# Performance work log

Hardware: AMD Instinct MI355X
Metric: run time of the kernel (lower is better)

The kernel has to match this reference:

```python
import jax, jax.numpy as jnp
import numpy as np

N_NODES = 100000
N_EDGES = 1600000


def _degree_norms(src, dst, n):
    ones = jnp.ones(src.shape[0], dtype=jnp.float32)
    deg_out = jax.ops.segment_sum(ones, src, num_segments=n)
    deg_in = jax.ops.segment_sum(ones, dst, num_segments=n)
    src_norm = jax.lax.rsqrt(jnp.maximum(deg_out, 1.0))
    dst_norm = jax.lax.rsqrt(jnp.maximum(deg_in, 1.0))
    return src_norm, dst_norm


def _graph_conv(x, W, b, src, dst, src_norm, dst_norm, n):
    # DGL GraphConv, norm='both': D_dst^{-1/2} A D_src^{-1/2} X W + b
    # Apply W first (same math, smaller messages).
    h = x @ W                                  # [N, out]
    m = (h * src_norm[:, None])[src]           # [E, out] gather
    agg = jax.ops.segment_sum(m, dst, num_segments=n)  # [N, out] scatter-add
    return agg * dst_norm[:, None] + b


def setup_inputs() -> dict:
    key = jax.random.key(0)
    ks = jax.random.split(key, 10)
    inp = {
        "x": jax.random.normal(ks[0], (N_NODES, 128), dtype=jnp.float32),
        "src": jax.random.randint(ks[1], (N_EDGES,), 0, N_NODES, dtype=jnp.int32),
        "dst": jax.random.randint(ks[2], (N_EDGES,), 0, N_NODES, dtype=jnp.int32),
        "W1": jax.random.normal(ks[3], (128, 64), dtype=jnp.float32) * 0.08,
        "b1": jnp.zeros((64,), dtype=jnp.float32),
        "W2": jax.random.normal(ks[4], (64, 64), dtype=jnp.float32) * 0.12,
        "b2": jnp.zeros((64,), dtype=jnp.float32),
        "W3": jax.random.normal(ks[5], (64, 64), dtype=jnp.float32) * 0.12,
        "b3": jnp.zeros((64,), dtype=jnp.float32),
        "W4": jax.random.normal(ks[6], (64, 64), dtype=jnp.float32) * 0.12,
        "b4": jnp.zeros((64,), dtype=jnp.float32),
        "Wres": jax.random.normal(ks[7], (128, 64), dtype=jnp.float32) * 0.08,
        "bres": jnp.zeros((64,), dtype=jnp.float32),
        "Wop": jax.random.normal(ks[8], (64, 16), dtype=jnp.float32) * 0.12,
        "bop": jnp.zeros((16,), dtype=jnp.float32),
    }
    return inp


def reference(x, src, dst, W1, b1, W2, b2, W3, b3, W4, b4, Wres, bres, Wop, bop):
    n = x.shape[0]
    src_norm, dst_norm = _degree_norms(src, dst, n)
    res = x @ Wres + bres
    out = jax.nn.relu(_graph_conv(x, W1, b1, src, dst, src_norm, dst_norm, n))
    out = jax.nn.relu(_graph_conv(out, W2, b2, src, dst, src_norm, dst_norm, n))
    out = jax.nn.relu(_graph_conv(out, W3, b3, src, dst, src_norm, dst_norm, n))
    out = _graph_conv(out, W4, b4, src, dst, src_norm, dst_norm, n)
    out = jax.nn.relu(out + res)
    return out @ Wop + bop
```

## Files before the change

### kernel.cpp

```cpp
#include <hip/hip_runtime.h>
#include <cstdint>
#include <cstddef>


#define SLOTS 64
#define BCAP 5120
#define ACHUNK 4096

__device__ __forceinline__ unsigned short f2bf(float f) {
  union { float f; unsigned u; } v; v.f = f;
  unsigned r = (v.u + 0x7fffu + ((v.u >> 16) & 1u)) >> 16;
  return (unsigned short)r;
}
__device__ __forceinline__ float bf2f(unsigned short h) {
  union { unsigned u; float f; } v; v.u = ((unsigned)h) << 16;
  return v.f;
}
__device__ __forceinline__ void bf2x2(unsigned u, float* lo, float* hi) {
  union { unsigned x; float f; } a, b;
  a.x = u << 16; b.x = u & 0xFFFF0000u;
  *lo = a.f; *hi = b.f;
}

__global__ __launch_bounds__(256) void bucket_kernel(
    const int* __restrict__ src, const int* __restrict__ dst,
    int* __restrict__ gcur_d, int* __restrict__ gcur_s,
    unsigned* __restrict__ dbuck, unsigned char* __restrict__ sbuck,
    int E, int nbuck) {
  __shared__ int s_src[ACHUNK];
  __shared__ int s_dst[ACHUNK];
  __shared__ int run_d[512];
  __shared__ int run_s[512];
  const int t = threadIdx.x;
  const int base = blockIdx.x * ACHUNK;
  int cnt = E - base;
  if (cnt > ACHUNK) cnt = ACHUNK;

  for (int i = t; i < cnt; i += 256) {
    s_src[i] = src[base + i];
    s_dst[i] = dst[base + i];
  }
  for (int i = t; i < nbuck; i += 256) { run_d[i] = 0; run_s[i] = 0; }
  __syncthreads();
  for (int i = t; i < cnt; i += 256) {
    atomicAdd(&run_d[s_dst[i] >> 8], 1);
    atomicAdd(&run_s[s_src[i] >> 8], 1);
  }
  __syncthreads();
  {
    const int iters = (nbuck + 255) >> 8;
    for (int it = 0; it < iters; ++it) {
      int i = it * 256 + t;
      int hd = 0, hs = 0;
      if (i < nbuck) { hd = run_d[i]; hs = run_s[i]; }
      __syncthreads();
      if (i < nbuck) {
        run_d[i] = hd ? atomicAdd(&gcur_d[i], hd) : 0;
        run_s[i] = hs ? atomicAdd(&gcur_s[i], hs) : 0;
      }
      __syncthreads();
    }
  }
  for (int i = t; i < cnt; i += 256) {
    int d = s_dst[i], s = s_src[i];
    int bd = d >> 8;
    int pd = atomicAdd(&run_d[bd], 1);
    if (pd < BCAP) dbuck[(size_t)bd * BCAP + pd] = ((unsigned)(d & 255) << 24) | (unsigned)s;
    int bs = s >> 8;
    int ps = atomicAdd(&run_s[bs], 1);
    if (ps < BCAP) sbuck[(size_t)bs * BCAP + ps] = (unsigned char)(s & 255);
  }
}

__global__ __launch_bounds__(256) void csr_kernel(
    const unsigned* __restrict__ dbuck, const int* __restrict__ gcur_d,
    int* __restrict__ col, int* __restrict__ cnt_arr,
    float* __restrict__ dnorm, int N) {
  __shared__ int cur[256];
  const int b = blockIdx.x;
  const int t = threadIdx.x;
  const int node0 = b << 8;
  cur[t] = 0;
  __syncthreads();
  int cnt = gcur_d[b];
  if (cnt > BCAP) cnt = BCAP;
  const unsigned* p = dbuck + (size_t)b * BCAP;
  for (int i = t; i < cnt; i += 256) {
    unsigned e = p[i];
    int nl = e >> 24;
    int s = (int)(e & 0x00FFFFFFu);
    int pos = atomicAdd(&cur[nl], 1);
    if (pos < SLOTS) col[(size_t)(node0 + nl) * SLOTS + pos] = s;
  }
  __syncthreads();
  int node = node0 + t;
  if (node < N) {
    int c = cur[t];
    cnt_arr[node] = c;
    float d = (float)(c < 1 ? 1 : c);
    dnorm[node] = rsqrtf(d);
  }
}

__global__ __launch_bounds__(256) void degout_kernel(
    const unsigned char* __restrict__ sbuck, const int* __restrict__ gcur_s,
    float* __restrict__ snorm, int N) {
  __shared__ int cur[256];
  const int b = blockIdx.x;
  const int t = threadIdx.x;
  cur[t] = 0;
  __syncthreads();
  int cnt = gcur_s[b];
  if (cnt > BCAP) cnt = BCAP;
  const unsigned char* p = sbuck + (size_t)b * BCAP;
  for (int i = t; i < cnt; i += 256) atomicAdd(&cur[p[i]], 1);
  __syncthreads();
  int node = (b << 8) + t;
  if (node < N) {
    int c = cur[t];
    snorm[node] = rsqrtf((float)(c < 1 ? 1 : c));
  }
}

#define GEMM_STEP(r, aval, wv)                   \
  acc[r][0] = fmaf((aval), (wv).x, acc[r][0]);   \
  acc[r][1] = fmaf((aval), (wv).y, acc[r][1]);   \
  acc[r][2] = fmaf((aval), (wv).z, acc[r][2]);   \
  acc[r][3] = fmaf((aval), (wv).w, acc[r][3]);

#define GEMM_INNER_LOOP                                        \
  for (int kc = 0; kc < 64; kc += 4) {                         \
    float4 a0 = *(const float4*)&in_lds[ty4 + 0][kc];          \
    float4 a1 = *(const float4*)&in_lds[ty4 + 1][kc];          \
    float4 a2 = *(const float4*)&in_lds[ty4 + 2][kc];          \
    float4 a3 = *(const float4*)&in_lds[ty4 + 3][kc];          \
    float4 w0 = *(const float4*)&w_lds[kc + 0][tx4];           \
    float4 w1 = *(const float4*)&w_lds[kc + 1][tx4];           \
    float4 w2 = *(const float4*)&w_lds[kc + 2][tx4];           \
    float4 w3 = *(const float4*)&w_lds[kc + 3][tx4];           \
    GEMM_STEP(0, a0.x, w0) GEMM_STEP(0, a0.y, w1) GEMM_STEP(0, a0.z, w2) GEMM_STEP(0, a0.w, w3) \
    GEMM_STEP(1, a1.x, w0) GEMM_STEP(1, a1.y, w1) GEMM_STEP(1, a1.z, w2) GEMM_STEP(1, a1.w, w3) \
    GEMM_STEP(2, a2.x, w0) GEMM_STEP(2, a2.y, w1) GEMM_STEP(2, a2.z, w2) GEMM_STEP(2, a2.w, w3) \
    GEMM_STEP(3, a3.x, w0) GEMM_STEP(3, a3.y, w1) GEMM_STEP(3, a3.z, w2) GEMM_STEP(3, a3.w, w3) \
  }

template <int K>
__global__ __launch_bounds__(256) void gemm_f32_kernel(
    const float* __restrict__ X, const float* __restrict__ W,
    const float* __restrict__ norm, unsigned short* __restrict__ out, int n) {
  __shared__ float in_lds[64][68];
  __shared__ float w_lds[64][64];
  const int t = threadIdx.x;
  const int tx4 = (t & 15) * 4;
  const int ty4 = (t >> 4) * 4;
  const int node0 = blockIdx.x * 64;
  const int srow = t >> 2;
  const int scol = (t & 3) * 16;

  float acc[4][4];
#pragma unroll
  for (int r = 0; r < 4; r++)
#pragma unroll
    for (int j = 0; j < 4; j++) acc[r][j] = 0.f;

  for (int kb = 0; kb < K; kb += 64) {
    {
      int gi = node0 + srow;
      float4 v0, v1, v2, v3;
      if (gi < n) {
        const float* s = X + (size_t)gi * K + kb + scol;
        v0 = *(const float4*)(s + 0);
        v1 = *(const float4*)(s + 4);
        v2 = *(const float4*)(s + 8);
        v3 = *(const float4*)(s + 12);
      } else {
        v0 = v1 = v2 = v3 = make_float4(0.f, 0.f, 0.f, 0.f);
      }
      *(float4*)&in_lds[srow][scol + 0]  = v0;
      *(float4*)&in_lds[srow][scol + 4]  = v1;
      *(float4*)&in_lds[srow][scol + 8]  = v2;
      *(float4*)&in_lds[srow][scol + 12] = v3;
    }
    {
      const float* s = W + (size_t)(kb + srow) * 64 + scol;
      float4 w0 = *(const float4*)(s + 0);
      float4 w1 = *(const float4*)(s + 4);
      float4 w2 = *(const float4*)(s + 8);
      float4 w3 = *(const float4*)(s + 12);
      *(float4*)&w_lds[srow][scol + 0]  = w0;
      *(float4*)&w_lds[srow][scol + 4]  = w1;
      *(float4*)&w_lds[srow][scol + 8]  = w2;
      *(float4*)&w_lds[srow][scol + 12] = w3;
    }
    __syncthreads();
    GEMM_INNER_LOOP
    __syncthreads();
  }

#pragma unroll
  for (int r = 0; r < 4; r++) {
    int gi = node0 + ty4 + r;
    if (gi >= n) continue;
    float s = norm[gi];
    ushort4 o;
    o.x = f2bf(acc[r][0] * s);
    o.y = f2bf(acc[r][1] * s);
    o.z = f2bf(acc[r][2] * s);
    o.w = f2bf(acc[r][3] * s);
    *(ushort4*)&out[(size_t)gi * 64 + tx4] = o;
  }
}

__global__ __launch_bounds__(256) void gemm_bf16_kernel(
    const unsigned short* __restrict__ X, const float* __restrict__ W,
    const float* __restrict__ norm, unsigned short* __restrict__ out, int n) {
  __shared__ float in_lds[64][68];
  __shared__ float w_lds[64][64];
  const int t = threadIdx.x;
  const int tx4 = (t & 15) * 4;
  const int ty4 = (t >> 4) * 4;
  const int node0 = blockIdx.x * 64;
  const int srow = t >> 2;
  const int scol = (t & 3) * 16;

  float acc[4][4];
#pragma unroll
  for (int r = 0; r < 4; r++)
#pragma unroll
    for (int j = 0; j < 4; j++) acc[r][j] = 0.f;

  {
    int gi = node0 + srow;
    float f[16];
    if (gi < n) {
      const unsigned short* s = X + (size_t)gi * 64 + scol;
      uint4 u0 = *(const uint4*)(s + 0);
      uint4 u1 = *(const uint4*)(s + 8);
      bf2x2(u0.x, &f[0], &f[1]);   bf2x2(u0.y, &f[2], &f[3]);
      bf2x2(u0.z, &f[4], &f[5]);   bf2x2(u0.w, &f[6], &f[7]);
      bf2x2(u1.x, &f[8], &f[9]);   bf2x2(u1.y, &f[10], &f[11]);
      bf2x2(u1.z, &f[12], &f[13]); bf2x2(u1.w, &f[14], &f[15]);
    } else {
#pragma unroll
      for (int j = 0; j < 16; j++) f[j] = 0.f;
    }
#pragma unroll
    for (int j = 0; j < 16; j += 4)
      *(float4*)&in_lds[srow][scol + j] = make_float4(f[j], f[j+1], f[j+2], f[j+3]);
  }
  {
    const float* s = W + (size_t)srow * 64 + scol;
    float4 w0 = *(const float4*)(s + 0);
    float4 w1 = *(const float4*)(s + 4);
    float4 w2 = *(const float4*)(s + 8);
    float4 w3 = *(const float4*)(s + 12);
    *(float4*)&w_lds[srow][scol + 0]  = w0;
    *(float4*)&w_lds[srow][scol + 4]  = w1;
    *(float4*)&w_lds[srow][scol + 8]  = w2;
    *(float4*)&w_lds[srow][scol + 12] = w3;
  }
  __syncthreads();
  GEMM_INNER_LOOP

#pragma unroll
  for (int r = 0; r < 4; r++) {
    int gi = node0 + ty4 + r;
    if (gi >= n) continue;
    float s = norm[gi];
    ushort4 o;
    o.x = f2bf(acc[r][0] * s);
    o.y = f2bf(acc[r][1] * s);
    o.z = f2bf(acc[r][2] * s);
    o.w = f2bf(acc[r][3] * s);
    *(ushort4*)&out[(size_t)gi * 64 + tx4] = o;
  }
}

#define UNPACK_ADD(u, A)                         \
  { float f0, f1, f2, f3;                        \
    bf2x2((u).x, &f0, &f1);                      \
    bf2x2((u).y, &f2, &f3);                      \
    A[0] += f0; A[1] += f1; A[2] += f2; A[3] += f3; }

template <int RELU>
__global__ __launch_bounds__(256) void agg_kernel(
    const unsigned short* __restrict__ H, const int* __restrict__ cnt_arr,
    const int* __restrict__ col, const float* __restrict__ dnorm,
    const float* __restrict__ bias, unsigned short* __restrict__ O,
    int n) {
  const int lane = threadIdx.x & 63;
  const int sub = lane >> 4;
  const int fl  = lane & 15;
  const int wave = (blockIdx.x * blockDim.x + threadIdx.x) >> 6;
  const int nwaves = (gridDim.x * blockDim.x) >> 6;
  const uint2* __restrict__ H2 = (const uint2*)H;
  const float4 bb = ((const float4*)bias)[fl];

  for (int v = wave; v < n; v += nwaves) {
    int cnt = cnt_arr[v];
    if (cnt > SLOTS) cnt = SLOTS;
    const size_t base = (size_t)v * SLOTS;
    int cv = (lane < cnt) ? col[base + lane] : 0;
    float accA[4] = {0.f, 0.f, 0.f, 0.f};
    float accB[4] = {0.f, 0.f, 0.f, 0.f};
    int j = 0;
    for (; j + 8 <= cnt; j += 8) {
      int c0 = __shfl(cv, j + sub);
      int c1 = __shfl(cv, j + 4 + sub);
      uint2 u0 = H2[(size_t)c0 * 16 + fl];
      uint2 u1 = H2[(size_t)c1 * 16 + fl];
      UNPACK_ADD(u0, accA)
      UNPACK_ADD(u1, accB)
    }
    for (; j < cnt; j += 4) {
      int e = j + sub;
      int c = __shfl(cv, e);
      if (e < cnt) {
        uint2 u = H2[(size_t)c * 16 + fl];
        UNPACK_ADD(u, accA)
      }
    }
#pragma unroll
    for (int i = 0; i < 4; i++) {
      float a = accA[i] + accB[i];
      a += __shfl_xor(a, 16);
      a += __shfl_xor(a, 32);
      accA[i] = a;
    }
    if (sub == 0) {
      float d = dnorm[v];
      float v0 = accA[0] * d + bb.x;
      float v1 = accA[1] * d + bb.y;
      float v2 = accA[2] * d + bb.z;
      float v3 = accA[3] * d + bb.w;
      if (RELU) {
        v0 = fmaxf(v0, 0.f); v1 = fmaxf(v1, 0.f);
        v2 = fmaxf(v2, 0.f); v3 = fmaxf(v3, 0.f);
      }
      ushort4 o;
      o.x = f2bf(v0); o.y = f2bf(v1); o.z = f2bf(v2); o.w = f2bf(v3);
      *(ushort4*)&O[base + 4 * fl] = o;
    }
  }
}

__global__ __launch_bounds__(256) void final_kernel(
    const float* __restrict__ X, const float* __restrict__ Wres,
    const float* __restrict__ bres, const unsigned short* __restrict__ O4,
    const float* __restrict__ Wop, const float* __restrict__ bop,
    float* __restrict__ out, int n) {
  __shared__ float in_lds[64][68];
  __shared__ float w_lds[64][64];
  __shared__ float wop_lds[64][16];
  const int t = threadIdx.x;
  const int tx4 = (t & 15) * 4;
  const int ty4 = (t >> 4) * 4;
  const int node0 = blockIdx.x * 64;
  const int srow = t >> 2;
  const int scol = (t & 3) * 16;

  ((float4*)&wop_lds[0][0])[t] = ((const float4*)Wop)[t];

  float acc[4][4];
#pragma unroll
  for (int r = 0; r < 4; r++)
#pragma unroll
    for (int j = 0; j < 4; j++) acc[r][j] = 0.f;

  for (int kb = 0; kb < 128; kb += 64) {
    {
      int gi = node0 + srow;
      float4 v0, v1, v2, v3;
      if (gi < n) {
        const float* s = X + (size_t)gi * 128 + kb + scol;
        v0 = *(const float4*)(s + 0);
        v1 = *(const float4*)(s + 4);
        v2 = *(const float4*)(s + 8);
        v3 = *(const float4*)(s + 12);
      } else {
        v0 = v1 = v2 = v3 = make_float4(0.f, 0.f, 0.f, 0.f);
      }
      *(float4*)&in_lds[srow][scol + 0]  = v0;
      *(float4*)&in_lds[srow][scol + 4]  = v1;
      *(float4*)&in_lds[srow][scol + 8]  = v2;
      *(float4*)&in_lds[srow][scol + 12] = v3;
    }
    {
      const float* s = Wres + (size_t)(kb + srow) * 64 + scol;
      float4 w0 = *(const float4*)(s + 0);
      float4 w1 = *(const float4*)(s + 4);
      float4 w2 = *(const float4*)(s + 8);
      float4 w3 = *(const float4*)(s + 12);
      *(float4*)&w_lds[srow][scol + 0]  = w0;
      *(float4*)&w_lds[srow][scol + 4]  = w1;
      *(float4*)&w_lds[srow][scol + 8]  = w2;
      *(float4*)&w_lds[srow][scol + 12] = w3;
    }
    __syncthreads();
    GEMM_INNER_LOOP
    __syncthreads();
  }

#pragma unroll
  for (int r = 0; r < 4; r++) {
    int gi = node0 + ty4 + r;
    float4 o = make_float4(0.f, 0.f, 0.f, 0.f);
    if (gi < n) {
      ushort4 v = *(const ushort4*)&O4[(size_t)gi * 64 + tx4];
      o.x = fmaxf(acc[r][0] + bres[tx4 + 0] + bf2f(v.x), 0.f);
      o.y = fmaxf(acc[r][1] + bres[tx4 + 1] + bf2f(v.y), 0.f);
      o.z = fmaxf(acc[r][2] + bres[tx4 + 2] + bf2f(v.z), 0.f);
      o.w = fmaxf(acc[r][3] + bres[tx4 + 3] + bf2f(v.w), 0.f);
    }
    *(float4*)&in_lds[ty4 + r][tx4] = o;
  }
  __syncthreads();

  {
    int nn = t >> 2;
    int fg = t & 3;
    float4 a = ((const float4*)bop)[fg];
#pragma unroll 16
    for (int k = 0; k < 64; k++) {
      float tv = in_lds[nn][k];
      float4 w = *(const float4*)&wop_lds[k][fg * 4];
      a.x = fmaf(tv, w.x, a.x);
      a.y = fmaf(tv, w.y, a.y);
      a.z = fmaf(tv, w.z, a.z);
      a.w = fmaf(tv, w.w, a.w);
    }
    int node = node0 + nn;
    if (node < n) *(float4*)&out[(size_t)node * 16 + fg * 4] = a;
  }
}

extern "C" void kernel_launch(void* const* d_in, const int* in_sizes, int n_in,
                              void* d_out, int out_size, void* d_ws, size_t ws_size,
                              hipStream_t stream) {
  const float* x    = (const float*)d_in[0];
  const int*   src  = (const int*)d_in[1];
  const int*   dst  = (const int*)d_in[2];
  const float* W1   = (const float*)d_in[3];
  const float* b1   = (const float*)d_in[4];
  const float* W2   = (const float*)d_in[5];
  const float* b2   = (const float*)d_in[6];
  const float* W3   = (const float*)d_in[7];
  const float* b3   = (const float*)d_in[8];
  const float* W4   = (const float*)d_in[9];
  const float* b4   = (const float*)d_in[10];
  const float* Wres = (const float*)d_in[11];
  const float* bres = (const float*)d_in[12];
  const float* Wop  = (const float*)d_in[13];
  const float* bop  = (const float*)d_in[14];
  float* out = (float*)d_out;

  const int N = in_sizes[0] / 128;
  const int E = in_sizes[1];
  const int nbuck = (N + 255) >> 8;

  char* p = (char*)d_ws;
  auto alloc = [&](size_t b) {
    char* r = p;
    p += (b + 255) & ~(size_t)255;
    return r;
  };
  int*            gcur_d  = (int*)alloc((size_t)nbuck * 4);
  int*            gcur_s  = (int*)alloc((size_t)nbuck * 4);
  unsigned*       dbuck   = (unsigned*)alloc((size_t)nbuck * BCAP * 4);
  unsigned char*  sbuck   = (unsigned char*)alloc((size_t)nbuck * BCAP);
  int*            col     = (int*)alloc((size_t)N * SLOTS * 4);
  int*            cnt_arr = (int*)alloc((size_t)N * 4);
  float*          snorm   = (float*)alloc((size_t)N * 4);
  float*          dnorm   = (float*)alloc((size_t)N * 4);
  unsigned short* Hbuf    = (unsigned short*)alloc((size_t)N * 64 * 2);
  unsigned short* Obuf    = (unsigned short*)alloc((size_t)N * 64 * 2);

  hipMemsetAsync(gcur_d, 0, (size_t)nbuck * 4, stream);
  hipMemsetAsync(gcur_s, 0, (size_t)nbuck * 4, stream);

  int ga = (E + ACHUNK - 1) / ACHUNK;
  bucket_kernel<<<ga, 256, 0, stream>>>(src, dst, gcur_d, gcur_s, dbuck, sbuck, E, nbuck);
  csr_kernel<<<nbuck, 256, 0, stream>>>(dbuck, gcur_d, col, cnt_arr, dnorm, N);
  degout_kernel<<<nbuck, 256, 0, stream>>>(sbuck, gcur_s, snorm, N);

  int gb = (N + 63) / 64;
  gemm_f32_kernel<128><<<gb, 256, 0, stream>>>(x, W1, snorm, Hbuf, N);
  agg_kernel<1><<<2048, 256, 0, stream>>>(Hbuf, cnt_arr, col, dnorm, b1, Obuf, N);
  gemm_bf16_kernel<<<gb, 256, 0, stream>>>(Obuf, W2, snorm, Hbuf, N);
  agg_kernel<1><<<2048, 256, 0, stream>>>(Hbuf, cnt_arr, col, dnorm, b2, Obuf, N);
  gemm_bf16_kernel<<<gb, 256, 0, stream>>>(Obuf, W3, snorm, Hbuf, N);
  agg_kernel<1><<<2048, 256, 0, stream>>>(Hbuf, cnt_arr, col, dnorm, b3, Obuf, N);
  gemm_bf16_kernel<<<gb, 256, 0, stream>>>(Obuf, W4, snorm, Hbuf, N);
  agg_kernel<0><<<2048, 256, 0, stream>>>(Hbuf, cnt_arr, col, dnorm, b4, Obuf, N);
  final_kernel<<<gb, 256, 0, stream>>>(x, Wres, bres, Obuf, Wop, bop, out, N);
}
```

Measured before the change: 325.7 us.

## Fuse residual GEMM into first GEMM and process two nodes per wave in aggregation

The residual projection x@Wres now happens in the first-layer GEMM kernel, which shares the x tile load with W1 and writes a bf16 residual buffer, so the final kernel no longer rereads x in fp32. The aggregation kernel now handles two destination nodes per wave and interleaves their gathers to raise memory-level parallelism. The two memsets become a single init kernel. In exchange the first GEMM uses more LDS and registers, the residual is rounded to bf16, and the aggregation loop runs to the larger of the two degrees with predicated loads.

Result: no change. 326.5 us (+0.3%).

```diff
diff --git a/kernel.cpp b/kernel.cpp
--- a/kernel.cpp
+++ b/kernel.cpp
@@ -20,6 +20,11 @@
   union { unsigned x; float f; } a, b;
   a.x = u << 16; b.x = u & 0xFFFF0000u;
   *lo = a.f; *hi = b.f;
+}
+
+__global__ void init_kernel(int* __restrict__ gcur_d, int* __restrict__ gcur_s, int nbuck) {
+  int i = blockIdx.x * blockDim.x + threadIdx.x;
+  if (i < nbuck) { gcur_d[i] = 0; gcur_s[i] = 0; }
 }
 
 __global__ __launch_bounds__(256) void bucket_kernel(
@@ -122,34 +127,41 @@
   }
 }
 
-#define GEMM_STEP(r, aval, wv)                   \
-  acc[r][0] = fmaf((aval), (wv).x, acc[r][0]);   \
-  acc[r][1] = fmaf((aval), (wv).y, acc[r][1]);   \
-  acc[r][2] = fmaf((aval), (wv).z, acc[r][2]);   \
-  acc[r][3] = fmaf((aval), (wv).w, acc[r][3]);
-
-#define GEMM_INNER_LOOP                                        \
-  for (int kc = 0; kc < 64; kc += 4) {                         \
-    float4 a0 = *(const float4*)&in_lds[ty4 + 0][kc];          \
-    float4 a1 = *(const float4*)&in_lds[ty4 + 1][kc];          \
-    float4 a2 = *(const float4*)&in_lds[ty4 + 2][kc];          \
-    float4 a3 = *(const float4*)&in_lds[ty4 + 3][kc];          \
-    float4 w0 = *(const float4*)&w_lds[kc + 0][tx4];           \
-    float4 w1 = *(const float4*)&w_lds[kc + 1][tx4];           \
-    float4 w2 = *(const float4*)&w_lds[kc + 2][tx4];           \
-    float4 w3 = *(const float4*)&w_lds[kc + 3][tx4];           \
-    GEMM_STEP(0, a0.x, w0) GEMM_STEP(0, a0.y, w1) GEMM_STEP(0, a0.z, w2) GEMM_STEP(0, a0.w, w3) \
-    GEMM_STEP(1, a1.x, w0) GEMM_STEP(1, a1.y, w1) GEMM_STEP(1, a1.z, w2) GEMM_STEP(1, a1.w, w3) \
-    GEMM_STEP(2, a2.x, w0) GEMM_STEP(2, a2.y, w1) GEMM_STEP(2, a2.z, w2) GEMM_STEP(2, a2.w, w3) \
-    GEMM_STEP(3, a3.x, w0) GEMM_STEP(3, a3.y, w1) GEMM_STEP(3, a3.z, w2) GEMM_STEP(3, a3.w, w3) \
-  }
-
-template <int K>
-__global__ __launch_bounds__(256) void gemm_f32_kernel(
-    const float* __restrict__ X, const float* __restrict__ W,
-    const float* __restrict__ norm, unsigned short* __restrict__ out, int n) {
+#define GEMM_STEP(ACC, r, aval, wv)                 \
+  ACC[r][0] = fmaf((aval), (wv).x, ACC[r][0]);      \
+  ACC[r][1] = fmaf((aval), (wv).y, ACC[r][1]);      \
+  ACC[r][2] = fmaf((aval), (wv).z, ACC[r][2]);      \
+  ACC[r][3] = fmaf((aval), (wv).w, ACC[r][3]);
+
+#define GEMM_ROW(ACC, W_LDS, kc)                                         \
+  { float4 w0 = *(const float4*)&W_LDS[kc + 0][tx4];                     \
+    float4 w1 = *(const float4*)&W_LDS[kc + 1][tx4];                     \
+    float4 w2 = *(const float4*)&W_LDS[kc + 2][tx4];                     \
+    float4 w3 = *(const float4*)&W_LDS[kc + 3][tx4];                     \
+    GEMM_STEP(ACC, 0, a0.x, w0) GEMM_STEP(ACC, 0, a0.y, w1) GEMM_STEP(ACC, 0, a0.z, w2) GEMM_STEP(ACC, 0, a0.w, w3) \
+    GEMM_STEP(ACC, 1, a1.x, w0) GEMM_STEP(ACC, 1, a1.y, w1) GEMM_STEP(ACC, 1, a1.z, w2) GEMM_STEP(ACC, 1, a1.w, w3) \
+    GEMM_STEP(ACC, 2, a2.x, w0) GEMM_STEP(ACC, 2, a2.y, w1) GEMM_STEP(ACC, 2, a2.z, w2) GEMM_STEP(ACC, 2, a2.w, w3) \
+    GEMM_STEP(ACC, 3, a3.x, w0) GEMM_STEP(ACC, 3, a3.y, w1) GEMM_STEP(ACC, 3, a3.z, w2) GEMM_STEP(ACC, 3, a3.w, w3) }
+
+#define STAGE_W_TILE(W_PTR, W_LDS)                                \
+  { const float* s_ = (W_PTR) + (size_t)srow * 64 + scol;         \
+    float4 q0 = *(const float4*)(s_ + 0);                         \
+    float4 q1 = *(const float4*)(s_ + 4);                         \
+    float4 q2 = *(const float4*)(s_ + 8);                         \
+    float4 q3 = *(const float4*)(s_ + 12);                        \
+    *(float4*)&W_LDS[srow][scol + 0]  = q0;                       \
+    *(float4*)&W_LDS[srow][scol + 4]  = q1;                       \
+    *(float4*)&W_LDS[srow][scol + 8]  = q2;                       \
+    *(float4*)&W_LDS[srow][scol + 12] = q3; }
+
+__global__ __launch_bounds__(256) void gemm1_kernel(
+    const float* __restrict__ X, const float* __restrict__ W1,
+    const float* __restrict__ Wres, const float* __restrict__ bres,
+    const float* __restrict__ norm,
+    unsigned short* __restrict__ Hout, unsigned short* __restrict__ Rout, int n) {
   __shared__ float in_lds[64][68];
   __shared__ float w_lds[64][64];
+  __shared__ float wr_lds[64][64];
   const int t = threadIdx.x;
   const int tx4 = (t & 15) * 4;
   const int ty4 = (t >> 4) * 4;
@@ -157,215 +169,11 @@
   const int srow = t >> 2;
   const int scol = (t & 3) * 16;
 
-  float acc[4][4];
+  float acc[4][4], acc2[4][4];
 #pragma unroll
   for (int r = 0; r < 4; r++)
 #pragma unroll
-    for (int j = 0; j < 4; j++) acc[r][j] = 0.f;
-
-  for (int kb = 0; kb < K; kb += 64) {
-    {
-      int gi = node0 + srow;
-      float4 v0, v1, v2, v3;
-      if (gi < n) {
-        const float* s = X + (size_t)gi * K + kb + scol;
-        v0 = *(const float4*)(s + 0);
-        v1 = *(const float4*)(s + 4);
-        v2 = *(const float4*)(s + 8);
-        v3 = *(const float4*)(s + 12);
-      } else {
-        v0 = v1 = v2 = v3 = make_float4(0.f, 0.f, 0.f, 0.f);
-      }
-      *(float4*)&in_lds[srow][scol + 0]  = v0;
-      *(float4*)&in_lds[srow][scol + 4]  = v1;
-      *(float4*)&in_lds[srow][scol + 8]  = v2;
-      *(float4*)&in_lds[srow][scol + 12] = v3;
-    }
-    {
-      const float* s = W + (size_t)(kb + srow) * 64 + scol;
-      float4 w0 = *(const float4*)(s + 0);
-      float4 w1 = *(const float4*)(s + 4);
-      float4 w2 = *(const float4*)(s + 8);
-      float4 w3 = *(const float4*)(s + 12);
-      *(float4*)&w_lds[srow][scol + 0]  = w0;
-      *(float4*)&w_lds[srow][scol + 4]  = w1;
-      *(float4*)&w_lds[srow][scol + 8]  = w2;
-      *(float4*)&w_lds[srow][scol + 12] = w3;
-    }
-    __syncthreads();
-    GEMM_INNER_LOOP
-    __syncthreads();
-  }
-
-#pragma unroll
-  for (int r = 0; r < 4; r++) {
-    int gi = node0 + ty4 + r;
-    if (gi >= n) continue;
-    float s = norm[gi];
-    ushort4 o;
-    o.x = f2bf(acc[r][0] * s);
-    o.y = f2bf(acc[r][1] * s);
-    o.z = f2bf(acc[r][2] * s);
-    o.w = f2bf(acc[r][3] * s);
-    *(ushort4*)&out[(size_t)gi * 64 + tx4] = o;
-  }
-}
-
-__global__ __launch_bounds__(256) void gemm_bf16_kernel(
-    const unsigned short* __restrict__ X, const float* __restrict__ W,
-    const float* __restrict__ norm, unsigned short* __restrict__ out, int n) {
-  __shared__ float in_lds[64][68];
-  __shared__ float w_lds[64][64];
-  const int t = threadIdx.x;
-  const int tx4 = (t & 15) * 4;
-  const int ty4 = (t >> 4) * 4;
-  const int node0 = blockIdx.x * 64;
-  const int srow = t >> 2;
-  const int scol = (t & 3) * 16;
-
-  float acc[4][4];
-#pragma unroll
-  for (int r = 0; r < 4; r++)
-#pragma unroll
-    for (int j = 0; j < 4; j++) acc[r][j] = 0.f;
-
-  {
-    int gi = node0 + srow;
-    float f[16];
-    if (gi < n) {
-      const unsigned short* s = X + (size_t)gi * 64 + scol;
-      uint4 u0 = *(const uint4*)(s + 0);
-      uint4 u1 = *(const uint4*)(s + 8);
-      bf2x2(u0.x, &f[0], &f[1]);   bf2x2(u0.y, &f[2], &f[3]);
-      bf2x2(u0.z, &f[4], &f[5]);   bf2x2(u0.w, &f[6], &f[7]);
-      bf2x2(u1.x, &f[8], &f[9]);   bf2x2(u1.y, &f[10], &f[11]);
-      bf2x2(u1.z, &f[12], &f[13]); bf2x2(u1.w, &f[14], &f[15]);
-    } else {
-#pragma unroll
-      for (int j = 0; j < 16; j++) f[j] = 0.f;
-    }
-#pragma unroll
-    for (int j = 0; j < 16; j += 4)
-      *(float4*)&in_lds[srow][scol + j] = make_float4(f[j], f[j+1], f[j+2], f[j+3]);
-  }
-  {
-    const float* s = W + (size_t)srow * 64 + scol;
-    float4 w0 = *(const float4*)(s + 0);
-    float4 w1 = *(const float4*)(s + 4);
-    float4 w2 = *(const float4*)(s + 8);
-    float4 w3 = *(const float4*)(s + 12);
-    *(float4*)&w_lds[srow][scol + 0]  = w0;
-    *(float4*)&w_lds[srow][scol + 4]  = w1;
-    *(float4*)&w_lds[srow][scol + 8]  = w2;
-    *(float4*)&w_lds[srow][scol + 12] = w3;
-  }
-  __syncthreads();
-  GEMM_INNER_LOOP
-
-#pragma unroll
-  for (int r = 0; r < 4; r++) {
-    int gi = node0 + ty4 + r;
-    if (gi >= n) continue;
-    float s = norm[gi];
-    ushort4 o;
-    o.x = f2bf(acc[r][0] * s);
-    o.y = f2bf(acc[r][1] * s);
-    o.z = f2bf(acc[r][2] * s);
-    o.w = f2bf(acc[r][3] * s);
-    *(ushort4*)&out[(size_t)gi * 64 + tx4] = o;
-  }
-}
-
-#define UNPACK_ADD(u, A)                         \
-  { float f0, f1, f2, f3;                        \
-    bf2x2((u).x, &f0, &f1);                      \
-    bf2x2((u).y, &f2, &f3);                      \
-    A[0] += f0; A[1] += f1; A[2] += f2; A[3] += f3; }
-
-template <int RELU>
-__global__ __launch_bounds__(256) void agg_kernel(
-    const unsigned short* __restrict__ H, const int* __restrict__ cnt_arr,
-    const int* __restrict__ col, const float* __restrict__ dnorm,
-    const float* __restrict__ bias, unsigned short* __restrict__ O,
-    int n) {
-  const int lane = threadIdx.x & 63;
-  const int sub = lane >> 4;
-  const int fl  = lane & 15;
-  const int wave = (blockIdx.x * blockDim.x + threadIdx.x) >> 6;
-  const int nwaves = (gridDim.x * blockDim.x) >> 6;
-  const uint2* __restrict__ H2 = (const uint2*)H;
-  const float4 bb = ((const float4*)bias)[fl];
-
-  for (int v = wave; v < n; v += nwaves) {
-    int cnt = cnt_arr[v];
-    if (cnt > SLOTS) cnt = SLOTS;
-    const size_t base = (size_t)v * SLOTS;
-    int cv = (lane < cnt) ? col[base + lane] : 0;
-    float accA[4] = {0.f, 0.f, 0.f, 0.f};
-    float accB[4] = {0.f, 0.f, 0.f, 0.f};
-    int j = 0;
-    for (; j + 8 <= cnt; j += 8) {
-      int c0 = __shfl(cv, j + sub);
-      int c1 = __shfl(cv, j + 4 + sub);
-      uint2 u0 = H2[(size_t)c0 * 16 + fl];
-      uint2 u1 = H2[(size_t)c1 * 16 + fl];
-      UNPACK_ADD(u0, accA)
-      UNPACK_ADD(u1, accB)
-    }
-    for (; j < cnt; j += 4) {
-      int e = j + sub;
-      int c = __shfl(cv, e);
-      if (e < cnt) {
-        uint2 u = H2[(size_t)c * 16 + fl];
-        UNPACK_ADD(u, accA)
-      }
-    }
-#pragma unroll
-    for (int i = 0; i < 4; i++) {
-      float a = accA[i] + accB[i];
-      a += __shfl_xor(a, 16);
-      a += __shfl_xor(a, 32);
-      accA[i] = a;
-    }
-    if (sub == 0) {
-      float d = dnorm[v];
-      float v0 = accA[0] * d + bb.x;
-      float v1 = accA[1] * d + bb.y;
-      float v2 = accA[2] * d + bb.z;
-      float v3 = accA[3] * d + bb.w;
-      if (RELU) {
-        v0 = fmaxf(v0, 0.f); v1 = fmaxf(v1, 0.f);
-        v2 = fmaxf(v2, 0.f); v3 = fmaxf(v3, 0.f);
-      }
-      ushort4 o;
-      o.x = f2bf(v0); o.y = f2bf(v1); o.z = f2bf(v2); o.w = f2bf(v3);
-      *(ushort4*)&O[base + 4 * fl] = o;
-    }
-  }
-}
-
-__global__ __launch_bounds__(256) void final_kernel(
-    const float* __restrict__ X, const float* __restrict__ Wres,
-    const float* __restrict__ bres, const unsigned short* __restrict__ O4,
-    const float* __restrict__ Wop, const float* __restrict__ bop,
-    float* __restrict__ out, int n) {
-  __shared__ float in_lds[64][68];
-  __shared__ float w_lds[64][64];
-  __shared__ float wop_lds[64][16];
-  const int t = threadIdx.x;
-  const int tx4 = (t & 15) * 4;
-  const int ty4 = (t >> 4) * 4;
-  const int node0 = blockIdx.x * 64;
-  const int srow = t >> 2;
-  const int scol = (t & 3) * 16;
-
-  ((float4*)&wop_lds[0][0])[t] = ((const float4*)Wop)[t];
-
-  float acc[4][4];
-#pragma unroll
-  for (int r = 0; r < 4; r++)
-#pragma unroll
-    for (int j = 0; j < 4; j++) acc[r][j] = 0.f;
+    for (int j = 0; j < 4; j++) { acc[r][j] = 0.f; acc2[r][j] = 0.f; }
 
   for (int kb = 0; kb < 128; kb += 64) {
     {
@@ -385,34 +193,232 @@
       *(float4*)&in_lds[srow][scol + 8]  = v2;
       *(float4*)&in_lds[srow][scol + 12] = v3;
     }
-    {
-      const float* s = Wres + (size_t)(kb + srow) * 64 + scol;
-      float4 w0 = *(const float4*)(s + 0);
-      float4 w1 = *(const float4*)(s + 4);
-      float4 w2 = *(const float4*)(s + 8);
-      float4 w3 = *(const float4*)(s + 12);
-      *(float4*)&w_lds[srow][scol + 0]  = w0;
-      *(float4*)&w_lds[srow][scol + 4]  = w1;
-      *(float4*)&w_lds[srow][scol + 8]  = w2;
-      *(float4*)&w_lds[srow][scol + 12] = w3;
-    }
+    STAGE_W_TILE(W1 + (size_t)kb * 64, w_lds)
+    STAGE_W_TILE(Wres + (size_t)kb * 64, wr_lds)
     __syncthreads();
-    GEMM_INNER_LOOP
+
+    for (int kc = 0; kc < 64; kc += 4) {
+      float4 a0 = *(const float4*)&in_lds[ty4 + 0][kc];
+      float4 a1 = *(const float4*)&in_lds[ty4 + 1][kc];
+      float4 a2 = *(const float4*)&in_lds[ty4 + 2][kc];
+      float4 a3 = *(const float4*)&in_lds[ty4 + 3][kc];
+      GEMM_ROW(acc, w_lds, kc)
+      GEMM_ROW(acc2, wr_lds, kc)
+    }
     __syncthreads();
   }
 
 #pragma unroll
   for (int r = 0; r < 4; r++) {
     int gi = node0 + ty4 + r;
-    float4 o = make_float4(0.f, 0.f, 0.f, 0.f);
+    if (gi >= n) continue;
+    float s = norm[gi];
+    ushort4 h;
+    h.x = f2bf(acc[r][0] * s);
+    h.y = f2bf(acc[r][1] * s);
+    h.z = f2bf(acc[r][2] * s);
+    h.w = f2bf(acc[r][3] * s);
+    *(ushort4*)&Hout[(size_t)gi * 64 + tx4] = h;
+    ushort4 rr;
+    rr.x = f2bf(acc2[r][0] + bres[tx4 + 0]);
+    rr.y = f2bf(acc2[r][1] + bres[tx4 + 1]);
+    rr.z = f2bf(acc2[r][2] + bres[tx4 + 2]);
+    rr.w = f2bf(acc2[r][3] + bres[tx4 + 3]);
+    *(ushort4*)&Rout[(size_t)gi * 64 + tx4] = rr;
+  }
+}
+
+__global__ __launch_bounds__(256) void gemm_bf16_kernel(
+    const unsigned short* __restrict__ X, const float* __restrict__ W,
+    const float* __restrict__ norm, unsigned short* __restrict__ out, int n) {
+  __shared__ float in_lds[64][68];
+  __shared__ float w_lds[64][64];
+  const int t = threadIdx.x;
+  const int tx4 = (t & 15) * 4;
+  const int ty4 = (t >> 4) * 4;
+  const int node0 = blockIdx.x * 64;
+  const int srow = t >> 2;
+  const int scol = (t & 3) * 16;
+
+  float acc[4][4];
+#pragma unroll
+  for (int r = 0; r < 4; r++)
+#pragma unroll
+    for (int j = 0; j < 4; j++) acc[r][j] = 0.f;
+
+  {
+    int gi = node0 + srow;
+    float f[16];
     if (gi < n) {
-      ushort4 v = *(const ushort4*)&O4[(size_t)gi * 64 + tx4];
-      o.x = fmaxf(acc[r][0] + bres[tx4 + 0] + bf2f(v.x), 0.f);
-      o.y = fmaxf(acc[r][1] + bres[tx4 + 1] + bf2f(v.y), 0.f);
-      o.z = fmaxf(acc[r][2] + bres[tx4 + 2] + bf2f(v.z), 0.f);
-      o.w = fmaxf(acc[r][3] + bres[tx4 + 3] + bf2f(v.w), 0.f);
-    }
-    *(float4*)&in_lds[ty4 + r][tx4] = o;
+      const unsigned short* s = X + (size_t)gi * 64 + scol;
+      uint4 u0 = *(const uint4*)(s + 0);
+      uint4 u1 = *(const uint4*)(s + 8);
+      bf2x2(u0.x, &f[0], &f[1]);   bf2x2(u0.y, &f[2], &f[3]);
+      bf2x2(u0.z, &f[4], &f[5]);   bf2x2(u0.w, &f[6], &f[7]);
+      bf2x2(u1.x, &f[8], &f[9]);   bf2x2(u1.y, &f[10], &f[11]);
+      bf2x2(u1.z, &f[12], &f[13]); bf2x2(u1.w, &f[14], &f[15]);
+    } else {
+#pragma unroll
+      for (int j = 0; j < 16; j++) f[j] = 0.f;
+    }
+#pragma unroll
+    for (int j = 0; j < 16; j += 4)
+      *(float4*)&in_lds[srow][scol + j] = make_float4(f[j], f[j+1], f[j+2], f[j+3]);
+  }
+  STAGE_W_TILE(W, w_lds)
+  __syncthreads();
+
+  for (int kc = 0; kc < 64; kc += 4) {
+    float4 a0 = *(const float4*)&in_lds[ty4 + 0][kc];
+    float4 a1 = *(const float4*)&in_lds[ty4 + 1][kc];
+    float4 a2 = *(const float4*)&in_lds[ty4 + 2][kc];
+    float4 a3 = *(const float4*)&in_lds[ty4 + 3][kc];
+    GEMM_ROW(acc, w_lds, kc)
+  }
+
+#pragma unroll
+  for (int r = 0; r < 4; r++) {
+    int gi = node0 + ty4 + r;
+    if (gi >= n) continue;
+    float s = norm[gi];
+    ushort4 o;
+    o.x = f2bf(acc[r][0] * s);
+    o.y = f2bf(acc[r][1] * s);
+    o.z = f2bf(acc[r][2] * s);
+    o.w = f2bf(acc[r][3] * s);
+    *(ushort4*)&out[(size_t)gi * 64 + tx4] = o;
+  }
+}
+
+#define UNPACK_ADD(u, A)                         \
+  { float f0, f1, f2, f3;                        \
+    bf2x2((u).x, &f0, &f1);                      \
+    bf2x2((u).y, &f2, &f3);                      \
+    A[0] += f0; A[1] += f1; A[2] += f2; A[3] += f3; }
+
+template <int RELU>
+__global__ __launch_bounds__(256) void agg_kernel(
+    const unsigned short* __restrict__ H, const int* __restrict__ cnt_arr,
+    const int* __restrict__ col, const float* __restrict__ dnorm,
+    const float* __restrict__ bias, unsigned short* __restrict__ O,
+    int n) {
+  const int lane = threadIdx.x & 63;
+  const int sub = lane >> 4;
+  const int fl  = lane & 15;
+  const int wave = (blockIdx.x * blockDim.x + threadIdx.x) >> 6;
+  const int nwaves = (gridDim.x * blockDim.x) >> 6;
+  const uint2* __restrict__ H2 = (const uint2*)H;
+  const float4 bb = ((const float4*)bias)[fl];
+
+  for (int v0 = wave * 2; v0 < n; v0 += nwaves * 2) {
+    const int v1 = v0 + 1;
+    int cnt0 = cnt_arr[v0];
+    int cnt1 = (v1 < n) ? cnt_arr[v1] : 0;
+    if (cnt0 > SLOTS) cnt0 = SLOTS;
+    if (cnt1 > SLOTS) cnt1 = SLOTS;
+    const size_t base0 = (size_t)v0 * SLOTS;
+    const size_t base1 = (size_t)v1 * SLOTS;
+    int cv0 = (lane < cnt0) ? col[base0 + lane] : 0;
+    int cv1 = (lane < cnt1) ? col[base1 + lane] : 0;
+    float a0[4] = {0.f, 0.f, 0.f, 0.f};
+    float b0[4] = {0.f, 0.f, 0.f, 0.f};
+    float a1[4] = {0.f, 0.f, 0.f, 0.f};
+    float b1[4] = {0.f, 0.f, 0.f, 0.f};
+    const int cmax = cnt0 > cnt1 ? cnt0 : cnt1;
+    for (int j = 0; j < cmax; j += 8) {
+      const int e0 = j + sub;
+      const int e1 = j + 4 + sub;
+      int c00 = __shfl(cv0, e0);
+      int c01 = __shfl(cv0, e1);
+      int c10 = __shfl(cv1, e0);
+      int c11 = __shfl(cv1, e1);
+      if (e0 < cnt0) { uint2 u = H2[(size_t)c00 * 16 + fl]; UNPACK_ADD(u, a0) }
+      if (e0 < cnt1) { uint2 u = H2[(size_t)c10 * 16 + fl]; UNPACK_ADD(u, a1) }
+      if (e1 < cnt0) { uint2 u = H2[(size_t)c01 * 16 + fl]; UNPACK_ADD(u, b0) }
+      if (e1 < cnt1) { uint2 u = H2[(size_t)c11 * 16 + fl]; UNPACK_ADD(u, b1) }
+    }
+    float r0[4], r1[4];
+#pragma unroll
+    for (int i = 0; i < 4; i++) {
+      float s0 = a0[i] + b0[i];
+      s0 += __shfl_xor(s0, 16);
+      s0 += __shfl_xor(s0, 32);
+      r0[i] = s0;
+      float s1 = a1[i] + b1[i];
+      s1 += __shfl_xor(s1, 16);
+      s1 += __shfl_xor(s1, 32);
+      r1[i] = s1;
+    }
+    if (sub == 0) {
+      float d = dnorm[v0];
+      float q0 = r0[0] * d + bb.x;
+      float q1 = r0[1] * d + bb.y;
+      float q2 = r0[2] * d + bb.z;
+      float q3 = r0[3] * d + bb.w;
+      if (RELU) {
+        q0 = fmaxf(q0, 0.f); q1 = fmaxf(q1, 0.f);
+        q2 = fmaxf(q2, 0.f); q3 = fmaxf(q3, 0.f);
+      }
+      ushort4 o;
+      o.x = f2bf(q0); o.y = f2bf(q1); o.z = f2bf(q2); o.w = f2bf(q3);
+      *(ushort4*)&O[base0 + 4 * fl] = o;
+    } else if (sub == 1 && v1 < n) {
+      float d = dnorm[v1];
+      float q0 = r1[0] * d + bb.x;
+      float q1 = r1[1] * d + bb.y;
+      float q2 = r1[2] * d + bb.z;
+      float q3 = r1[3] * d + bb.w;
+      if (RELU) {
+        q0 = fmaxf(q0, 0.f); q1 = fmaxf(q1, 0.f);
+        q2 = fmaxf(q2, 0.f); q3 = fmaxf(q3, 0.f);
+      }
+      ushort4 o;
+      o.x = f2bf(q0); o.y = f2bf(q1); o.z = f2bf(q2); o.w = f2bf(q3);
+      *(ushort4*)&O[base1 + 4 * fl] = o;
+    }
+  }
+}
+
+__global__ __launch_bounds__(256) void final_kernel(
+    const unsigned short* __restrict__ O4, const unsigned short* __restrict__ R,
+    const float* __restrict__ Wop, const float* __restrict__ bop,
+    float* __restrict__ out, int n) {
+  __shared__ float t_lds[64][68];
+  __shared__ float wop_lds[64][16];
+  const int t = threadIdx.x;
+  const int node0 = blockIdx.x * 64;
+  const int srow = t >> 2;
+  const int scol = (t & 3) * 16;
+
+  ((float4*)&wop_lds[0][0])[t] = ((const float4*)Wop)[t];
+
+  {
+    int gi = node0 + srow;
+    float f[16];
+    if (gi < n) {
+      const unsigned short* po = O4 + (size_t)gi * 64 + scol;
+      const unsigned short* pr = R + (size_t)gi * 64 + scol;
+      uint4 uo0 = *(const uint4*)(po + 0);
+      uint4 uo1 = *(const uint4*)(po + 8);
+      uint4 ur0 = *(const uint4*)(pr + 0);
+      uint4 ur1 = *(const uint4*)(pr + 8);
+      float o0, o1, rr0, rr1;
+#define ADDRELU2(UO, UR, idx)                         \
+      bf2x2(UO, &o0, &o1); bf2x2(UR, &rr0, &rr1);     \
+      f[idx] = fmaxf(o0 + rr0, 0.f);                  \
+      f[idx + 1] = fmaxf(o1 + rr1, 0.f);
+      ADDRELU2(uo0.x, ur0.x, 0)  ADDRELU2(uo0.y, ur0.y, 2)
+      ADDRELU2(uo0.z, ur0.z, 4)  ADDRELU2(uo0.w, ur0.w, 6)
+      ADDRELU2(uo1.x, ur1.x, 8)  ADDRELU2(uo1.y, ur1.y, 10)
+      ADDRELU2(uo1.z, ur1.z, 12) ADDRELU2(uo1.w, ur1.w, 14)
+#undef ADDRELU2
+    } else {
+#pragma unroll
+      for (int j = 0; j < 16; j++) f[j] = 0.f;
+    }
+#pragma unroll
+    for (int j = 0; j < 16; j += 4)
+      *(float4*)&t_lds[srow][scol + j] = make_float4(f[j], f[j+1], f[j+2], f[j+3]);
   }
   __syncthreads();
 
@@ -422,7 +428,7 @@
     float4 a = ((const float4*)bop)[fg];
 #pragma unroll 16
     for (int k = 0; k < 64; k++) {
-      float tv = in_lds[nn][k];
+      float tv = t_lds[nn][k];
       float4 w = *(const float4*)&wop_lds[k][fg * 4];
       a.x = fmaf(tv, w.x, a.x);
       a.y = fmaf(tv, w.y, a.y);
@@ -474,9 +480,9 @@
   float*          dnorm   = (float*)alloc((size_t)N * 4);
   unsigned short* Hbuf    = (unsigned short*)alloc((size_t)N * 64 * 2);
   unsigned short* Obuf    = (unsigned short*)alloc((size_t)N * 64 * 2);
-
-  hipMemsetAsync(gcur_d, 0, (size_t)nbuck * 4, stream);
-  hipMemsetAsync(gcur_s, 0, (size_t)nbuck * 4, stream);
+  unsigned short* Rbuf    = (unsigned short*)alloc((size_t)N * 64 * 2);
+
+  init_kernel<<<(nbuck + 255) / 256, 256, 0, stream>>>(gcur_d, gcur_s, nbuck);
 
   int ga = (E + ACHUNK - 1) / ACHUNK;
   bucket_kernel<<<ga, 256, 0, stream>>>(src, dst, gcur_d, gcur_s, dbuck, sbuck, E, nbuck);
@@ -484,7 +490,7 @@
   degout_kernel<<<nbuck, 256, 0, stream>>>(sbuck, gcur_s, snorm, N);
 
   int gb = (N + 63) / 64;
-  gemm_f32_kernel<128><<<gb, 256, 0, stream>>>(x, W1, snorm, Hbuf, N);
+  gemm1_kernel<<<gb, 256, 0, stream>>>(x, W1, Wres, bres, snorm, Hbuf, Rbuf, N);
   agg_kernel<1><<<2048, 256, 0, stream>>>(Hbuf, cnt_arr, col, dnorm, b1, Obuf, N);
   gemm_bf16_kernel<<<gb, 256, 0, stream>>>(Obuf, W2, snorm, Hbuf, N);
   agg_kernel<1><<<2048, 256, 0, stream>>>(Hbuf, cnt_arr, col, dnorm, b2, Obuf, N);
@@ -492,5 +498,5 @@
   agg_kernel<1><<<2048, 256, 0, stream>>>(Hbuf, cnt_arr, col, dnorm, b3, Obuf, N);
   gemm_bf16_kernel<<<gb, 256, 0, stream>>>(Obuf, W4, snorm, Hbuf, N);
   agg_kernel<0><<<2048, 256, 0, stream>>>(Hbuf, cnt_arr, col, dnorm, b4, Obuf, N);
-  final_kernel<<<gb, 256, 0, stream>>>(x, Wres, bres, Obuf, Wop, bop, out, N);
-}
+  final_kernel<<<gb, 256, 0, stream>>>(Obuf, Rbuf, Wop, bop, out, N);
+}
```
